# Optimization experiments

Measured on AMD Instinct MI355X. Metric: run time of the kernel, lower is better.

Reference implementation:

```python
import jax, jax.numpy as jnp
import numpy as np


def setup_inputs() -> dict:
    key = jax.random.key(0)
    ks = jax.random.split(key, 6)
    B, M, H = 256, 64, 512
    memory_state = jax.random.normal(ks[0], (B, M, M, M), dtype=jnp.float32) * 0.02
    hidden_state = jax.random.normal(ks[1], (B, H), dtype=jnp.float32)
    role1 = jnp.tanh(jax.random.normal(ks[2], (B, M), dtype=jnp.float32))
    role2 = jnp.tanh(jax.random.normal(ks[3], (B, M), dtype=jnp.float32))
    filer = jnp.tanh(jax.random.normal(ks[4], (B, M), dtype=jnp.float32))
    W_gate = jax.random.normal(ks[5], (1, H), dtype=jnp.float32) * (1.0 / np.sqrt(H))
    b_gate = jnp.zeros((1,), dtype=jnp.float32)
    return {"memory_state": memory_state, "hidden_state": hidden_state,
            "role1": role1, "role2": role2, "filer": filer,
            "W_gate": W_gate, "b_gate": b_gate}


def reference(memory_state, hidden_state, role1, role2, filer, W_gate, b_gate):
    M = memory_state.shape[1]
    # write gate: sigmoid(Linear(h) + 1), shape [B, 1]
    write_gate = jax.nn.sigmoid(hidden_state @ W_gate.T + b_gate + 1.0)
    # outer product of roles: [B, M, M]
    role = jnp.einsum('br,bt->brt', role1, role2)
    # read from 3D associative memory: [B, M]
    prev_info = jnp.einsum('brt,brtf->bf', role, memory_state)
    cur_info = write_gate * (filer - prev_info)
    scale = 1.0 / M
    # gated outer-product write
    new_memory = memory_state + jnp.einsum('brt,bf->brtf', role, cur_info * scale)
    # norm-clip rescale
    mem_norm = jnp.linalg.norm(new_memory.reshape(new_memory.shape[0], -1), axis=-1)
    mem_norm = jax.nn.relu(mem_norm - 1.0) + 1.0
    new_memory = new_memory / mem_norm[:, None, None, None]
    return new_memory
```

## Files before the change

kernel.cpp:

```cpp
#include <hip/hip_runtime.h>
#include <math.h>

#define M 64
#define B 256
#define T 256

__device__ __forceinline__ float wave_sum64(float v) {
    #pragma unroll
    for (int m = 32; m >= 1; m >>= 1) v += __shfl_xor(v, m);
    return v;
}

__global__ __launch_bounds__(T) void k_reduce(
    const float* __restrict__ mem, const float* __restrict__ role1,
    const float* __restrict__ role2, float* __restrict__ prev_part,
    float* __restrict__ ss_part)
{
    const int b   = blockIdx.x >> 3;
    const int sp  = blockIdx.x & 7;
    const int tid = threadIdx.x;

    __shared__ float  role_s[512];
    __shared__ float4 part[4][16];
    __shared__ float  ss_lds[4];

    for (int i = tid; i < 512; i += T) {
        const int rt = sp * 512 + i;
        role_s[i] = role1[b * M + (rt >> 6)] * role2[b * M + (rt & 63)];
    }
    __syncthreads();

    const float4* mem4 = (const float4*)(mem + (size_t)b * 262144);
    const int f4 = tid & 15, rsub = tid >> 4;

    float4 ap = make_float4(0.f, 0.f, 0.f, 0.f);
    float  ss = 0.f;
    #pragma unroll 8
    for (int i = 0; i < 32; ++i) {
        const int lrt = rsub + i * 16;
        const float4 v = mem4[(sp * 512 + lrt) * 16 + f4];
        const float  r = role_s[lrt];
        ap.x = fmaf(r, v.x, ap.x);
        ap.y = fmaf(r, v.y, ap.y);
        ap.z = fmaf(r, v.z, ap.z);
        ap.w = fmaf(r, v.w, ap.w);
        ss = fmaf(v.x, v.x, ss);
        ss = fmaf(v.y, v.y, ss);
        ss = fmaf(v.z, v.z, ss);
        ss = fmaf(v.w, v.w, ss);
    }

    #pragma unroll
    for (int m = 16; m <= 32; m <<= 1) {
        ap.x += __shfl_xor(ap.x, m);
        ap.y += __shfl_xor(ap.y, m);
        ap.z += __shfl_xor(ap.z, m);
        ap.w += __shfl_xor(ap.w, m);
    }
    const float ssw = wave_sum64(ss);

    const int wave = tid >> 6, lane = tid & 63;
    if (lane < 16) part[wave][lane] = ap;
    if (lane == 0) ss_lds[wave] = ssw;
    __syncthreads();

    if (tid < 16) {
        float4 a0 = part[0][tid], a1 = part[1][tid], a2 = part[2][tid], a3 = part[3][tid];
        float4 s;
        s.x = (a0.x + a1.x) + (a2.x + a3.x);
        s.y = (a0.y + a1.y) + (a2.y + a3.y);
        s.z = (a0.z + a1.z) + (a2.z + a3.z);
        s.w = (a0.w + a1.w) + (a2.w + a3.w);
        ((float4*)prev_part)[(size_t)(b * 8 + sp) * 16 + tid] = s;
    }
    if (tid == 0)
        ss_part[b * 8 + sp] = (ss_lds[0] + ss_lds[1]) + (ss_lds[2] + ss_lds[3]);
}

__global__ __launch_bounds__(T) void k_write(
    const float* __restrict__ mem, const float* __restrict__ hidden,
    const float* __restrict__ role1, const float* __restrict__ role2,
    const float* __restrict__ filer, const float* __restrict__ W_gate,
    const float* __restrict__ b_gate, const float* __restrict__ prev_part,
    const float* __restrict__ ss_part, float* __restrict__ out)
{
    const int b   = blockIdx.x >> 3;
    const int sp  = blockIdx.x & 7;
    const int tid = threadIdx.x;

    __shared__ float role_s[512];
    __shared__ float c2_s[M];
    __shared__ float inv_s;

    if (tid < M) {
        const int f = tid;
        float p = 0.f;
        #pragma unroll
        for (int s = 0; s < 8; ++s) p += prev_part[(size_t)(b * 8 + s) * M + f];
        float ssm = 0.f;
        #pragma unroll
        for (int s = 0; s < 8; ++s) ssm += ss_part[b * 8 + s];

        float g = 0.f;
        #pragma unroll
        for (int j = 0; j < 8; ++j)
            g = fmaf(hidden[(size_t)b * 512 + f + j * 64], W_gate[f + j * 64], g);
        g = wave_sum64(g);
        g = 1.f / (1.f + expf(-(g + b_gate[0] + 1.f)));

        const float fil = filer[b * M + f];
        const float cur = g * (fil - p);
        const float d1   = wave_sum64(p * cur);
        const float ssc  = wave_sum64(cur * cur);
        const float r1   = role1[b * M + f];
        const float r2   = role2[b * M + f];
        const float ssr1 = wave_sum64(r1 * r1);
        const float ssr2 = wave_sum64(r2 * r2);

        const float sc = 1.0f / (float)M;
        const float ns = ssm + 2.f * sc * d1 + sc * sc * ssr1 * ssr2 * ssc;
        const float inv = 1.0f / fmaxf(sqrtf(ns), 1.0f);
        c2_s[f] = cur * sc * inv;
        if (f == 0) inv_s = inv;
    }
    for (int i = tid; i < 512; i += T) {
        const int rt = sp * 512 + i;
        role_s[i] = role1[b * M + (rt >> 6)] * role2[b * M + (rt & 63)];
    }
    __syncthreads();

    const float  inv = inv_s;
    const float4 c   = ((const float4*)c2_s)[tid & 15];
    const float4* mem4 = (const float4*)(mem + (size_t)b * 262144);
    float4* out4 = (float4*)(out + (size_t)b * 262144);
    const int f4 = tid & 15, rsub = tid >> 4;

    #pragma unroll 8
    for (int i = 0; i < 32; ++i) {
        const int lrt = rsub + i * 16;
        const int idx = (sp * 512 + lrt) * 16 + f4;
        const float4 v = mem4[idx];
        const float  r = role_s[lrt];
        float4 o;
        o.x = fmaf(r, c.x, v.x * inv);
        o.y = fmaf(r, c.y, v.y * inv);
        o.z = fmaf(r, c.z, v.z * inv);
        o.w = fmaf(r, c.w, v.w * inv);
        out4[idx] = o;
    }
}

extern "C" void kernel_launch(void* const* d_in, const int* in_sizes, int n_in,
                              void* d_out, int out_size, void* d_ws, size_t ws_size,
                              hipStream_t stream) {
    const float* mem    = (const float*)d_in[0];
    const float* hidden = (const float*)d_in[1];
    const float* role1  = (const float*)d_in[2];
    const float* role2  = (const float*)d_in[3];
    const float* filer  = (const float*)d_in[4];
    const float* Wg     = (const float*)d_in[5];
    const float* bg     = (const float*)d_in[6];
    float* out = (float*)d_out;

    float* ws        = (float*)d_ws;
    float* prev_part = ws;
    float* ss_part   = ws + 131072;

    hipLaunchKernelGGL(k_reduce, dim3(B * 8), dim3(T), 0, stream,
                       mem, role1, role2, prev_part, ss_part);
    hipLaunchKernelGGL(k_write, dim3(B * 8), dim3(T), 0, stream,
                       mem, hidden, role1, role2, filer, Wg, bg,
                       prev_part, ss_part, out);
}
```

Before: 164.0 us.

## Chunk batches across reduce/write launches so second memory read hits cache

Splits the batch into four chunks and runs the reduce and write kernels per chunk, so each chunk's memory state may still be resident in the last-level cache when the write pass rereads it. Slices per batch double to 16 with smaller row tiles and fully unrolled loops. The write pass uses nontemporal loads for the final read. This adds extra kernel launches and smaller grids per launch, which may add launch overhead and reduce parallelism.

After: 177.4 us. 8.2% more time.

```diff
diff --git a/kernel.cpp b/kernel.cpp
--- a/kernel.cpp
+++ b/kernel.cpp
@@ -4,6 +4,12 @@
 #define M 64
 #define B 256
 #define T 256
+#define SLICES 16
+#define ROWS 256
+#define CHUNK 64
+#define NCHUNK 4
+
+typedef float f32x4 __attribute__((ext_vector_type(4)));
 
 __device__ __forceinline__ float wave_sum64(float v) {
     #pragma unroll
@@ -14,18 +20,18 @@
 __global__ __launch_bounds__(T) void k_reduce(
     const float* __restrict__ mem, const float* __restrict__ role1,
     const float* __restrict__ role2, float* __restrict__ prev_part,
-    float* __restrict__ ss_part)
+    float* __restrict__ ss_part, int b0)
 {
-    const int b   = blockIdx.x >> 3;
-    const int sp  = blockIdx.x & 7;
+    const int b   = b0 + (blockIdx.x >> 4);
+    const int sl  = blockIdx.x & 15;
     const int tid = threadIdx.x;
 
-    __shared__ float  role_s[512];
+    __shared__ float  role_s[ROWS];
     __shared__ float4 part[4][16];
     __shared__ float  ss_lds[4];
 
-    for (int i = tid; i < 512; i += T) {
-        const int rt = sp * 512 + i;
+    for (int i = tid; i < ROWS; i += T) {
+        const int rt = sl * ROWS + i;
         role_s[i] = role1[b * M + (rt >> 6)] * role2[b * M + (rt & 63)];
     }
     __syncthreads();
@@ -35,10 +41,10 @@
 
     float4 ap = make_float4(0.f, 0.f, 0.f, 0.f);
     float  ss = 0.f;
-    #pragma unroll 8
-    for (int i = 0; i < 32; ++i) {
-        const int lrt = rsub + i * 16;
-        const float4 v = mem4[(sp * 512 + lrt) * 16 + f4];
+    #pragma unroll
+    for (int i = 0; i < 16; ++i) {
+        const int lrt = i * 16 + rsub;
+        const float4 v = mem4[(sl * ROWS + lrt) * 16 + f4];
         const float  r = role_s[lrt];
         ap.x = fmaf(r, v.x, ap.x);
         ap.y = fmaf(r, v.y, ap.y);
@@ -71,10 +77,10 @@
         s.y = (a0.y + a1.y) + (a2.y + a3.y);
         s.z = (a0.z + a1.z) + (a2.z + a3.z);
         s.w = (a0.w + a1.w) + (a2.w + a3.w);
-        ((float4*)prev_part)[(size_t)(b * 8 + sp) * 16 + tid] = s;
+        ((float4*)prev_part)[(size_t)(b * SLICES + sl) * 16 + tid] = s;
     }
     if (tid == 0)
-        ss_part[b * 8 + sp] = (ss_lds[0] + ss_lds[1]) + (ss_lds[2] + ss_lds[3]);
+        ss_part[b * SLICES + sl] = (ss_lds[0] + ss_lds[1]) + (ss_lds[2] + ss_lds[3]);
 }
 
 __global__ __launch_bounds__(T) void k_write(
@@ -82,13 +88,13 @@
     const float* __restrict__ role1, const float* __restrict__ role2,
     const float* __restrict__ filer, const float* __restrict__ W_gate,
     const float* __restrict__ b_gate, const float* __restrict__ prev_part,
-    const float* __restrict__ ss_part, float* __restrict__ out)
+    const float* __restrict__ ss_part, float* __restrict__ out, int b0)
 {
-    const int b   = blockIdx.x >> 3;
-    const int sp  = blockIdx.x & 7;
+    const int b   = b0 + (blockIdx.x >> 4);
+    const int sl  = blockIdx.x & 15;
     const int tid = threadIdx.x;
 
-    __shared__ float role_s[512];
+    __shared__ float role_s[ROWS];
     __shared__ float c2_s[M];
     __shared__ float inv_s;
 
@@ -96,10 +102,11 @@
         const int f = tid;
         float p = 0.f;
         #pragma unroll
-        for (int s = 0; s < 8; ++s) p += prev_part[(size_t)(b * 8 + s) * M + f];
+        for (int s = 0; s < SLICES; ++s)
+            p += prev_part[(size_t)(b * SLICES + s) * M + f];
         float ssm = 0.f;
         #pragma unroll
-        for (int s = 0; s < 8; ++s) ssm += ss_part[b * 8 + s];
+        for (int s = 0; s < SLICES; ++s) ssm += ss_part[b * SLICES + s];
 
         float g = 0.f;
         #pragma unroll
@@ -123,29 +130,29 @@
         c2_s[f] = cur * sc * inv;
         if (f == 0) inv_s = inv;
     }
-    for (int i = tid; i < 512; i += T) {
-        const int rt = sp * 512 + i;
+    for (int i = tid; i < ROWS; i += T) {
+        const int rt = sl * ROWS + i;
         role_s[i] = role1[b * M + (rt >> 6)] * role2[b * M + (rt & 63)];
     }
     __syncthreads();
 
     const float  inv = inv_s;
-    const float4 c   = ((const float4*)c2_s)[tid & 15];
-    const float4* mem4 = (const float4*)(mem + (size_t)b * 262144);
+    const float4 cc  = ((const float4*)c2_s)[tid & 15];
+    const f32x4* mem4 = (const f32x4*)(mem + (size_t)b * 262144);
     float4* out4 = (float4*)(out + (size_t)b * 262144);
     const int f4 = tid & 15, rsub = tid >> 4;
 
-    #pragma unroll 8
-    for (int i = 0; i < 32; ++i) {
-        const int lrt = rsub + i * 16;
-        const int idx = (sp * 512 + lrt) * 16 + f4;
-        const float4 v = mem4[idx];
-        const float  r = role_s[lrt];
+    #pragma unroll
+    for (int i = 0; i < 16; ++i) {
+        const int lrt = i * 16 + rsub;
+        const int idx = (sl * ROWS + lrt) * 16 + f4;
+        const f32x4 v = __builtin_nontemporal_load(&mem4[idx]);
+        const float r = role_s[lrt];
         float4 o;
-        o.x = fmaf(r, c.x, v.x * inv);
-        o.y = fmaf(r, c.y, v.y * inv);
-        o.z = fmaf(r, c.z, v.z * inv);
-        o.w = fmaf(r, c.w, v.w * inv);
+        o.x = fmaf(r, cc.x, v.x * inv);
+        o.y = fmaf(r, cc.y, v.y * inv);
+        o.z = fmaf(r, cc.z, v.z * inv);
+        o.w = fmaf(r, cc.w, v.w * inv);
         out4[idx] = o;
     }
 }
@@ -164,11 +171,14 @@
 
     float* ws        = (float*)d_ws;
     float* prev_part = ws;
-    float* ss_part   = ws + 131072;
+    float* ss_part   = ws + 262144;
 
-    hipLaunchKernelGGL(k_reduce, dim3(B * 8), dim3(T), 0, stream,
-                       mem, role1, role2, prev_part, ss_part);
-    hipLaunchKernelGGL(k_write, dim3(B * 8), dim3(T), 0, stream,
-                       mem, hidden, role1, role2, filer, Wg, bg,
-                       prev_part, ss_part, out);
+    for (int c = 0; c < NCHUNK; ++c) {
+        const int b0 = c * CHUNK;
+        hipLaunchKernelGGL(k_reduce, dim3(CHUNK * SLICES), dim3(T), 0, stream,
+                           mem, role1, role2, prev_part, ss_part, b0);
+        hipLaunchKernelGGL(k_write, dim3(CHUNK * SLICES), dim3(T), 0, stream,
+                           mem, hidden, role1, role2, filer, Wg, bg,
+                           prev_part, ss_part, out, b0);
+    }
 }
```
